# Kernel tuning notes

Hardware: AMD Instinct MI355X
Metric: run time of the kernel (lower is better)

The kernel has to match this reference:

```python
import jax, jax.numpy as jnp
import numpy as np

EPS = 1e-6


def _rmsnorm(x, w, eps=EPS):
    # x: (..., d); normalize over last dim
    ms = jnp.mean(jnp.square(x), axis=-1, keepdims=True)
    return x * jax.lax.rsqrt(ms + eps) * w


def setup_inputs() -> dict:
    key = jax.random.key(0)
    ks = jax.random.split(key, 5)
    B, S, D = 2, 2048, 2048
    n_heads, n_kv = 16, 4
    d_head = D // n_heads  # 128
    sd = 1.0 / np.sqrt(D)
    return {
        "x": jax.random.normal(ks[0], (B, S, D), dtype=jnp.float32),
        "wq": jax.random.normal(ks[1], (D, n_heads * d_head), dtype=jnp.float32) * sd,
        "wk": jax.random.normal(ks[2], (D, n_kv * d_head), dtype=jnp.float32) * sd,
        "wv": jax.random.normal(ks[3], (D, n_kv * d_head), dtype=jnp.float32) * sd,
        "wo": jax.random.normal(ks[4], (D, D), dtype=jnp.float32) * sd,
        "q_norm_w": jnp.ones((d_head,), dtype=jnp.float32),
        "k_norm_w": jnp.ones((d_head,), dtype=jnp.float32),
    }


def reference(x, wq, wk, wv, wo, q_norm_w, k_norm_w):
    B, S, D = x.shape
    n_heads, n_kv = 16, 4
    groups = n_heads // n_kv
    d_head = D // n_heads

    # QKV projections (bias=False)
    q = (x @ wq).reshape(B, S, n_kv, groups, d_head)  # q heads grouped by kv head
    k = (x @ wk).reshape(B, S, n_kv, d_head)
    v = (x @ wv).reshape(B, S, n_kv, d_head)

    # qk RMSNorm over d_head
    q = _rmsnorm(q, q_norm_w)
    k = _rmsnorm(k, k_norm_w)

    # GQA attention without materializing expanded K/V:
    # scores: (B, n_kv, groups, S_q, S_k)
    scale = 1.0 / jnp.sqrt(jnp.asarray(d_head, dtype=x.dtype))
    scores = jnp.einsum('bskgd,btkd->bkgst', q, k) * scale
    causal = jnp.tril(jnp.ones((S, S), dtype=bool))
    scores = jnp.where(causal, scores, jnp.asarray(-jnp.inf, dtype=scores.dtype))
    attn = jax.nn.softmax(scores, axis=-1)
    out = jnp.einsum('bkgst,btkd->bskgd', attn, v)  # (B, S, n_kv, groups, d_head)
    out = out.reshape(B, S, D)
    return out @ wo
```

## Files before the change

kernel.cpp:

```cpp
#include <hip/hip_runtime.h>
#include <hip/hip_bf16.h>
#include <stdint.h>

typedef unsigned short u16;
typedef __attribute__((ext_vector_type(8))) short short8;
typedef __attribute__((ext_vector_type(4))) float f32x4;
typedef __attribute__((ext_vector_type(16))) float f32x16;

__device__ __forceinline__ u16 f2bf(float f){
  union { __hip_bfloat16 h; u16 u; } v; v.h = __float2bfloat16(f); return v.u;
}
__device__ __forceinline__ float bf2f(u16 h){
  union { uint32_t u; float f; } v; v.u = ((uint32_t)h) << 16;
  return v.f;
}
__device__ __forceinline__ f32x4 mfma16(short8 a, short8 b, f32x4 c){
  return __builtin_amdgcn_mfma_f32_16x16x32_bf16(a, b, c, 0, 0, 0);
}
__device__ __forceinline__ f32x16 mfma32(short8 a, short8 b, f32x16 c){
  return __builtin_amdgcn_mfma_f32_32x32x16_bf16(a, b, c, 0, 0, 0);
}
__device__ __forceinline__ void gl_lds16(const u16* g, u16* l){
  __builtin_amdgcn_global_load_lds((const __attribute__((address_space(1))) void*)g,
                                   (__attribute__((address_space(3))) void*)l, 16, 0, 0);
}
template<int N> __device__ __forceinline__ void waitvm(){
  if constexpr (N==0) asm volatile("s_waitcnt vmcnt(0)" ::: "memory");
  else if constexpr (N==4) asm volatile("s_waitcnt vmcnt(4)" ::: "memory");
  else static_assert(N==0 || N==4, "unsupported vmcnt");
}
__device__ __forceinline__ void phase_sep(){
  __builtin_amdgcn_sched_barrier(0);
  __builtin_amdgcn_s_barrier();
  __builtin_amdgcn_sched_barrier(0);
}

__global__ __launch_bounds__(256) void cvt_x(const float* __restrict__ s,
                                             u16* __restrict__ d, int n4){
  const int i = blockIdx.x*256 + threadIdx.x;
  if (i >= n4) return;
  const float4 v = ((const float4*)s)[i];
  ushort4 pk;
  pk.x = f2bf(v.x); pk.y = f2bf(v.y); pk.z = f2bf(v.z); pk.w = f2bf(v.w);
  ((ushort4*)d)[i] = pk;
}

__global__ __launch_bounds__(256) void transpose_cvt(const float* __restrict__ src,
    u16* __restrict__ dst, int R, int C)
{
  __shared__ float tile[32][33];
  const int tx = threadIdx.x, ty = threadIdx.y;
  const int c0 = blockIdx.x << 5, r0 = blockIdx.y << 5;
  #pragma unroll
  for (int i=0;i<4;i++)
    tile[ty + (i<<3)][tx] = src[(size_t)(r0 + ty + (i<<3))*C + c0 + tx];
  __syncthreads();
  #pragma unroll
  for (int i=0;i<4;i++)
    dst[(size_t)(c0 + ty + (i<<3))*R + r0 + tx] = f2bf(tile[tx][ty + (i<<3)]);
}

__global__ __launch_bounds__(256) void v_transpose(const u16* __restrict__ qkv,
    u16* __restrict__ vT)
{
  __shared__ u16 tile[32][33];
  const int tx = threadIdx.x, ty = threadIdx.y;
  const int s0 = blockIdx.x << 5, d0 = blockIdx.y << 5;
  const int bk = blockIdx.z; const int b = bk >> 2, kv = bk & 3;
  const u16* src = qkv + (size_t)b*2048*3072 + 2560 + kv*128;
  #pragma unroll
  for (int i=0;i<4;i++)
    tile[ty + (i<<3)][tx] = src[(size_t)(s0 + ty + (i<<3))*3072 + d0 + tx];
  __syncthreads();
  u16* dst = vT + (size_t)((b<<2)+kv)*128*2048;
  #pragma unroll
  for (int i=0;i<4;i++)
    dst[(size_t)(d0 + ty + (i<<3))*2048 + s0 + tx] = tile[tx][ty + (i<<3)];
}

__global__ __launch_bounds__(256) void rmsnorm_qk(u16* __restrict__ qkv,
    const float* __restrict__ qw, const float* __restrict__ kw)
{
  const int lane = threadIdx.x & 63;
  const int rid = blockIdx.x*4 + (threadIdx.x >> 6);
  const int row = rid / 20;
  const int slot = rid % 20;
  u16* p = qkv + (size_t)row*3072 + slot*128 + (lane<<1);
  const u16 r0 = p[0], r1 = p[1];
  const float a = bf2f(r0), c = bf2f(r1);
  float ss = a*a + c*c;
  #pragma unroll
  for (int off=1; off<64; off<<=1) ss += __shfl_xor(ss, off);
  float sc = rsqrtf(ss*(1.0f/128.0f) + 1e-6f);
  if (slot < 16) sc *= 0.1275187952317199f;
  const float* wp = (slot < 16) ? qw : kw;
  const float w0 = wp[lane<<1], w1 = wp[(lane<<1)+1];
  p[0] = f2bf(a*sc*w0);
  p[1] = f2bf(c*sc*w1);
}

template<int CBF16>
__global__ __launch_bounds__(512, 2) void gemm8(const u16* __restrict__ A,
    const u16* __restrict__ BT, void* __restrict__ Cp,
    int M, int N, int K, int ldc)
{
  __shared__ u16 lds[65536];
  const int tid = threadIdx.x;
  const int w = tid >> 6, lane = tid & 63;
  const int l15 = lane & 15, lg = lane >> 4;
  const int wm = w >> 2, wn = w & 3;
  const int nbx = N >> 8;
  const int nwg = gridDim.x;
  int bid = blockIdx.x;
  bid = (bid & 7) * (nwg >> 3) + (bid >> 3);
  const int m0 = (bid / nbx) << 8;
  const int n0 = (bid % nbx) << 8;

  const u16* gA0 = A  + (size_t)m0*K;
  const u16* gA1 = gA0 + (size_t)128*K;
  const u16* gB0 = BT + (size_t)n0*K;
  const u16* gB1 = gB0 + (size_t)128*K;

  auto slot = [&](int d, int s)->u16*{ return lds + (((d<<2)+s)<<13); };

  auto stage_half = [&](const u16* gbase, int kt, u16* sbase){
    #pragma unroll
    for (int i=0;i<2;i++){
      const int p = (i<<9) + tid;
      const int row = p>>3, sg = (p&7) ^ (row&7);
      gl_lds16(gbase + (size_t)row*K + (kt<<6) + (sg<<3), sbase + (p<<3));
    }
  };
  auto frag_at = [&](const u16* buf, int lrow, int kk)->short8{
    const int s = ((kk<<2)+lg) ^ (lrow&7);
    return *(const short8*)(buf + (((lrow<<3)+s)<<3));
  };

  short8 af[4][2], bfe[2][2], bfo[2][2];
  f32x4 acc[8][4];
  #pragma unroll
  for (int m=0;m<8;m++)
    #pragma unroll
    for (int n=0;n<4;n++) acc[m][n] = (f32x4){0.f,0.f,0.f,0.f};

  const int bh = 2 + (wn>>1);
  const int brow0 = ((wn&1)<<6) + l15;

  auto rd_a = [&](const u16* buf, int mq){
    #pragma unroll
    for (int m=0;m<4;m++)
      #pragma unroll
      for (int kk=0;kk<2;kk++)
        af[m][kk] = frag_at(buf, (mq<<6) + (m<<4) + l15, kk);
  };
  auto rd_b = [&](const u16* buf, int nq, short8 (*dst)[2]){
    #pragma unroll
    for (int n=0;n<2;n++)
      #pragma unroll
      for (int kk=0;kk<2;kk++)
        dst[n][kk] = frag_at(buf, brow0 + (nq<<5) + (n<<4), kk);
  };
  auto do_mfma = [&](int mb, int nb, short8 (*bf)[2]){
    __builtin_amdgcn_s_setprio(1);
    #pragma unroll
    for (int m=0;m<4;m++)
      #pragma unroll
      for (int n=0;n<2;n++)
        #pragma unroll
        for (int kk=0;kk<2;kk++)
          acc[mb+m][nb+n] = mfma16(af[m][kk], bf[n][kk], acc[mb+m][nb+n]);
    __builtin_amdgcn_s_setprio(0);
  };

  stage_half(gA0, 0, slot(0,0)); stage_half(gA1, 0, slot(0,1));
  stage_half(gB0, 0, slot(0,2)); stage_half(gB1, 0, slot(0,3));
  stage_half(gA0, 1, slot(1,0)); stage_half(gA1, 1, slot(1,1));
  waitvm<4>();
  phase_sep();

  const int niter = K >> 7;
  for (int i=0; i<niter; ++i){
    const bool full = (i+1 < niter);
    const int t1 = 2*i+1;
    rd_a(slot(0,wm), 0); rd_b(slot(0,bh), 0, bfe);
    stage_half(gB0, t1, slot(1,2)); stage_half(gB1, t1, slot(1,3));
    phase_sep();
    do_mfma(0, 0, bfe);
    phase_sep();
    rd_b(slot(0,bh), 1, bfo);
    phase_sep();
    do_mfma(0, 2, bfo);
    phase_sep();
    rd_a(slot(0,wm), 1);
    phase_sep();
    do_mfma(4, 2, bfo);
    phase_sep();
    rd_b(slot(0,bh), 0, bfe);
    if (full){ stage_half(gA0, t1+1, slot(0,0)); stage_half(gA1, t1+1, slot(0,1)); }
    phase_sep();
    do_mfma(4, 0, bfe);
    if (full) waitvm<4>(); else waitvm<0>();
    phase_sep();
    rd_a(slot(1,wm), 0); rd_b(slot(1,bh), 0, bfe);
    if (full){ stage_half(gB0, t1+1, slot(0,2)); stage_half(gB1, t1+1, slot(0,3)); }
    phase_sep();
    do_mfma(0, 0, bfe);
    phase_sep();
    rd_b(slot(1,bh), 1, bfo);
    phase_sep();
    do_mfma(0, 2, bfo);
    phase_sep();
    rd_a(slot(1,wm), 1);
    phase_sep();
    do_mfma(4, 2, bfo);
    phase_sep();
    rd_b(slot(1,bh), 0, bfe);
    if (full){ stage_half(gA0, t1+2, slot(1,0)); stage_half(gA1, t1+2, slot(1,1)); }
    phase_sep();
    do_mfma(4, 0, bfe);
    if (full) waitvm<4>();
    phase_sep();
  }

  #pragma unroll
  for (int m=0;m<8;m++){
    #pragma unroll
    for (int n=0;n<4;n++){
      const int col = n0 + (wn<<6) + (n<<4) + l15;
      #pragma unroll
      for (int r=0;r<4;r++){
        const int row = m0 + (wm<<7) + (m<<4) + (lg<<2) + r;
        if (CBF16) ((u16*)Cp)[(size_t)row*ldc + col] = f2bf(acc[m][n][r]);
        else       ((float*)Cp)[(size_t)row*ldc + col] = acc[m][n][r];
      }
    }
  }
}

__global__ __launch_bounds__(512, 2) void attn_kernel(const u16* __restrict__ qkv,
    const u16* __restrict__ vT, u16* __restrict__ aout)
{
  __shared__ u16 Klds[2][8192];
  __shared__ u16 Vlds[2][8192];
  __shared__ u16 Plds[8][2048];
  const int tid = threadIdx.x;
  const int w = tid >> 6, lane = tid & 63;
  const int l31 = lane & 31, hi = lane >> 5;
  const int P = blockIdx.x;
  const int h = blockIdx.y, b = blockIdx.z;
  const int kvh = h >> 2;
  const int side = w >> 2, sub = w & 3;
  const int qb = (side ? P*128 : (15-P)*128) + (sub<<5);
  const int nt = 32 - 2*P;
  const int ltmax = 2*P + 1;

  const u16* qkvb = qkv + (size_t)b*2048*3072;
  short8 qf[8];
  {
    const u16* qp = qkvb + (size_t)(qb + l31)*3072 + h*128 + hi*8;
    #pragma unroll
    for (int kk=0;kk<8;kk++) qf[kk] = *(const short8*)(qp + kk*16);
  }
  f32x16 oacc[4];
  #pragma unroll
  for (int d=0;d<4;d++)
    #pragma unroll
    for (int r=0;r<16;r++) oacc[d][r] = 0.f;
  float m_run = -__builtin_inff(), lsum = 0.f;

  const u16* kb_ = qkvb + 2048 + kvh*128;
  const u16* vb_ = vT + (size_t)((b<<2)+kvh)*128*2048;

  auto stageKV = [&](int t, int buf){
    const int t0s = t<<6;
    #pragma unroll
    for (int i=0;i<2;i++){
      const int u = (i<<9) + tid;
      const int row = u>>4, d0 = (u&15) ^ (row&15);
      gl_lds16(kb_ + (size_t)(t0s+row)*3072 + (d0<<3), &Klds[buf][u<<3]);
    }
    #pragma unroll
    for (int i=0;i<2;i++){
      const int u = (i<<9) + tid;
      const int rp = u>>4, z = (u&15) ^ (rp&15);
      const int d = (rp<<1) + (z>>3), k8 = z&7;
      gl_lds16(vb_ + (size_t)d*2048 + t0s + (k8<<3), &Vlds[buf][u<<3]);
    }
  };

  u16* Pw = &Plds[w][0];
  const int prp = l31>>1;

  stageKV(0, 0);
  asm volatile("s_waitcnt vmcnt(0)" ::: "memory");
  __syncthreads();

  int cur = 0;
  for (int t=0; t<nt; ++t){
    if (t+1 < nt) stageKV(t+1, cur^1);
    const int t0 = t<<6;
    const bool active = (side ? (t <= ltmax) : true) && (t0 <= qb + 31);
    if (active){
      f32x16 s0, s1;
      #pragma unroll
      for (int r=0;r<16;r++){ s0[r] = 0.f; s1[r] = 0.f; }
      #pragma unroll
      for (int kk=0;kk<8;kk++){
        const int d0 = (kk<<1) + hi;
        const int row0 = l31,     sl0 = d0 ^ (row0&15);
        const int row1 = 32+l31,  sl1 = d0 ^ (row1&15);
        const short8 k0 = *(const short8*)&Klds[cur][((row0<<4)+sl0)<<3];
        s0 = mfma32(k0, qf[kk], s0);
        const short8 k1 = *(const short8*)&Klds[cur][((row1<<4)+sl1)<<3];
        s1 = mfma32(k1, qf[kk], s1);
      }
      if (t0 + 63 > qb){
        const int qrel = qb + l31 - t0;
        #pragma unroll
        for (int r=0;r<16;r++){
          const int kloc = (r&3) + ((r>>2)<<3) + (hi<<2);
          if (kloc      > qrel) s0[r] = -__builtin_inff();
          if (kloc + 32 > qrel) s1[r] = -__builtin_inff();
        }
      }
      float t8[8];
      #pragma unroll
      for (int i=0;i<8;i++) t8[i] = fmaxf(fmaxf(s0[i], s0[i+8]), fmaxf(s1[i], s1[i+8]));
      #pragma unroll
      for (int i=0;i<4;i++) t8[i] = fmaxf(t8[i], t8[i+4]);
      float mx = fmaxf(fmaxf(t8[0],t8[1]), fmaxf(t8[2],t8[3]));
      mx = fmaxf(mx, __shfl_xor(mx, 32));
      const bool noskip = !__all(mx - m_run <= 8.0f);
      const float mnew = noskip ? fmaxf(m_run, mx) : m_run;
      float rs = 0.f;
      #pragma unroll
      for (int i=0;i<16;i++){
        s0[i] = __builtin_amdgcn_exp2f(s0[i] - mnew);
        s1[i] = __builtin_amdgcn_exp2f(s1[i] - mnew);
        rs += s0[i] + s1[i];
      }
      rs += __shfl_xor(rs, 32);
      if (noskip){
        const float corr = __builtin_amdgcn_exp2f(m_run - mnew);
        m_run = mnew;
        lsum = lsum*corr + rs;
        #pragma unroll
        for (int r=0;r<16;r++){
          const float cr = __shfl(corr, (r&3) + ((r>>2)<<3) + (hi<<2));
          #pragma unroll
          for (int db=0;db<4;db++) oacc[db][r] *= cr;
        }
      } else {
        lsum += rs;
      }
      #pragma unroll
      for (int kb2=0;kb2<2;kb2++)
        #pragma unroll
        for (int j=0;j<4;j++){
          const int r4 = j<<2;
          uint2 v;
          if (kb2==0){
            v.x = (uint32_t)f2bf(s0[r4+0]) | ((uint32_t)f2bf(s0[r4+1])<<16);
            v.y = (uint32_t)f2bf(s0[r4+2]) | ((uint32_t)f2bf(s0[r4+3])<<16);
          } else {
            v.x = (uint32_t)f2bf(s1[r4+0]) | ((uint32_t)f2bf(s1[r4+1])<<16);
            v.y = (uint32_t)f2bf(s1[r4+2]) | ((uint32_t)f2bf(s1[r4+3])<<16);
          }
          const int sl = (((l31&1)<<3) | ((kb2<<2)+j)) ^ (prp&15);
          *(uint2*)((char*)Pw + ((((prp<<4)+sl)<<4) + (hi<<3))) = v;
        }
      asm volatile("s_waitcnt lgkmcnt(0)" ::: "memory");
      __builtin_amdgcn_sched_barrier(0);
      #pragma unroll
      for (int kk=0;kk<4;kk++){
        const int k8 = (kk<<1) + hi;
        const int slp = (((l31&1)<<3) | k8) ^ (prp&15);
        const short8 pa = *(const short8*)&Pw[((prp<<4)+slp)<<3];
        #pragma unroll
        for (int db=0;db<4;db++){
          const int d = (db<<5) + l31;
          const int rp = d>>1;
          const int slv = (((d&1)<<3) | k8) ^ (rp&15);
          const short8 vv = *(const short8*)&Vlds[cur][((rp<<4)+slv)<<3];
          oacc[db] = mfma32(pa, vv, oacc[db]);
        }
      }
    }
    asm volatile("s_waitcnt vmcnt(0)" ::: "memory");
    __syncthreads();
    cur ^= 1;
  }

  const float inv = 1.0f / lsum;
  #pragma unroll
  for (int r=0;r<16;r++){
    const int qr = (r&3) + ((r>>2)<<3) + (hi<<2);
    const float ivr = __shfl(inv, qr);
    u16* op = aout + (size_t)(b*2048 + qb + qr)*2048 + h*128 + l31;
    #pragma unroll
    for (int db=0;db<4;db++)
      op[db<<5] = f2bf(oacc[db][r] * ivr);
  }
}

extern "C" void kernel_launch(void* const* d_in, const int* in_sizes, int n_in,
                              void* d_out, int out_size, void* d_ws, size_t ws_size,
                              hipStream_t stream) {
  const float* x  = (const float*)d_in[0];
  const float* wq = (const float*)d_in[1];
  const float* wk = (const float*)d_in[2];
  const float* wv = (const float*)d_in[3];
  const float* wo = (const float*)d_in[4];
  const float* qw = (const float*)d_in[5];
  const float* kw = (const float*)d_in[6];
  char* ws = (char*)d_ws;
  u16* xbf   = (u16*)(ws);
  u16* wqkvT = (u16*)(ws + 16777216);
  u16* woT   = (u16*)(ws + 29360128);
  u16* qkv   = (u16*)(ws + 37748736);
  u16* vT    = (u16*)(ws + 62914560);
  float* out = (float*)d_out;

  dim3 tb(32,8);
  cvt_x<<<8192, 256, 0, stream>>>(x, xbf, 2097152);
  transpose_cvt<<<dim3(64,64), tb, 0, stream>>>(wq, wqkvT,             2048, 2048);
  transpose_cvt<<<dim3(16,64), tb, 0, stream>>>(wk, wqkvT + 2048*2048, 2048, 512);
  transpose_cvt<<<dim3(16,64), tb, 0, stream>>>(wv, wqkvT + 2560*2048, 2048, 512);
  transpose_cvt<<<dim3(64,64), tb, 0, stream>>>(wo, woT,               2048, 2048);
  gemm8<1><<<192, 512, 0, stream>>>(xbf, wqkvT, qkv, 4096, 3072, 2048, 3072);
  rmsnorm_qk<<<20480, 256, 0, stream>>>(qkv, qw, kw);
  v_transpose<<<dim3(64,4,8), tb, 0, stream>>>(qkv, vT);
  attn_kernel<<<dim3(8,16,2), 512, 0, stream>>>(qkv, vT, xbf);
  gemm8<0><<<128, 512, 0, stream>>>(xbf, woT, out, 4096, 2048, 2048, 2048);
}
```

Measured before the change: 215.9 us.

## Restructure attention into 256-thread blocks with register-resident P and split K/V staging

The attention kernel moves from 512-thread blocks that pair two query tiles to 256-thread blocks each owning one 128-row query tile. The grid doubles and the light/heavy ordering is flipped by batch index. The P matrix no longer round-trips through LDS. It is packed in registers with v_cvt_pk_bf16_f32 and rearranged across lanes with v_permlane32_swap to form the MFMA A operand. K stays double-buffered while V is single-buffered and loaded each tile, with staged vmcnt waits and barriers to overlap the next K load with compute. This removes LDS traffic and the lgkm wait for P, but adds an extra barrier per tile and exposes V load latency.

```diff
diff --git a/kernel.cpp b/kernel.cpp
--- a/kernel.cpp
+++ b/kernel.cpp
@@ -27,12 +27,18 @@
 template<int N> __device__ __forceinline__ void waitvm(){
   if constexpr (N==0) asm volatile("s_waitcnt vmcnt(0)" ::: "memory");
   else if constexpr (N==4) asm volatile("s_waitcnt vmcnt(4)" ::: "memory");
-  else static_assert(N==0 || N==4, "unsupported vmcnt");
+  else if constexpr (N==8) asm volatile("s_waitcnt vmcnt(8)" ::: "memory");
+  else static_assert(N==0 || N==4 || N==8, "unsupported vmcnt");
 }
 __device__ __forceinline__ void phase_sep(){
   __builtin_amdgcn_sched_barrier(0);
   __builtin_amdgcn_s_barrier();
   __builtin_amdgcn_sched_barrier(0);
+}
+__device__ __forceinline__ uint32_t cvtpk(float lo, float hi){
+  uint32_t r;
+  asm("v_cvt_pk_bf16_f32 %0, %1, %2" : "=v"(r) : "v"(lo), "v"(hi));
+  return r;
 }
 
 __global__ __launch_bounds__(256) void cvt_x(const float* __restrict__ s,
@@ -237,22 +243,19 @@
   }
 }
 
-__global__ __launch_bounds__(512, 2) void attn_kernel(const u16* __restrict__ qkv,
+__global__ __launch_bounds__(256, 2) void attn_kernel(const u16* __restrict__ qkv,
     const u16* __restrict__ vT, u16* __restrict__ aout)
 {
   __shared__ u16 Klds[2][8192];
-  __shared__ u16 Vlds[2][8192];
-  __shared__ u16 Plds[8][2048];
+  __shared__ u16 Vlds[8192];
   const int tid = threadIdx.x;
   const int w = tid >> 6, lane = tid & 63;
   const int l31 = lane & 31, hi = lane >> 5;
-  const int P = blockIdx.x;
-  const int h = blockIdx.y, b = blockIdx.z;
+  const int bx = blockIdx.x, h = blockIdx.y, b = blockIdx.z;
+  const int qI = b ? bx : (15 - bx);
   const int kvh = h >> 2;
-  const int side = w >> 2, sub = w & 3;
-  const int qb = (side ? P*128 : (15-P)*128) + (sub<<5);
-  const int nt = 32 - 2*P;
-  const int ltmax = 2*P + 1;
+  const int qb = qI*128 + (w<<5);
+  const int nt = 2*qI + 2;
 
   const u16* qkvb = qkv + (size_t)b*2048*3072;
   short8 qf[8];
@@ -271,47 +274,46 @@
   const u16* kb_ = qkvb + 2048 + kvh*128;
   const u16* vb_ = vT + (size_t)((b<<2)+kvh)*128*2048;
 
-  auto stageKV = [&](int t, int buf){
-    const int t0s = t<<6;
-    #pragma unroll
-    for (int i=0;i<2;i++){
-      const int u = (i<<9) + tid;
+  auto stageK = [&](int t, int buf){
+    #pragma unroll
+    for (int i=0;i<4;i++){
+      const int u = (i<<8) + tid;
       const int row = u>>4, d0 = (u&15) ^ (row&15);
-      gl_lds16(kb_ + (size_t)(t0s+row)*3072 + (d0<<3), &Klds[buf][u<<3]);
-    }
-    #pragma unroll
-    for (int i=0;i<2;i++){
-      const int u = (i<<9) + tid;
+      gl_lds16(kb_ + (size_t)((t<<6)+row)*3072 + (d0<<3), &Klds[buf][u<<3]);
+    }
+  };
+  auto stageV = [&](int t){
+    #pragma unroll
+    for (int i=0;i<4;i++){
+      const int u = (i<<8) + tid;
       const int rp = u>>4, z = (u&15) ^ (rp&15);
       const int d = (rp<<1) + (z>>3), k8 = z&7;
-      gl_lds16(vb_ + (size_t)d*2048 + t0s + (k8<<3), &Vlds[buf][u<<3]);
-    }
-  };
-
-  u16* Pw = &Plds[w][0];
-  const int prp = l31>>1;
-
-  stageKV(0, 0);
-  asm volatile("s_waitcnt vmcnt(0)" ::: "memory");
-  __syncthreads();
-
-  int cur = 0;
+      gl_lds16(vb_ + (size_t)d*2048 + (t<<6) + (k8<<3), &Vlds[u<<3]);
+    }
+  };
+
+  stageK(0, 0);
+  int kbuf = 0;
   for (int t=0; t<nt; ++t){
-    if (t+1 < nt) stageKV(t+1, cur^1);
+    const bool pre = (t+1 < nt);
+    stageV(t);
+    if (pre) stageK(t+1, kbuf^1);
+    if (pre) waitvm<8>(); else waitvm<4>();
+    phase_sep();
     const int t0 = t<<6;
-    const bool active = (side ? (t <= ltmax) : true) && (t0 <= qb + 31);
-    if (active){
+    const bool act = (t0 <= qb + 31);
+    uint32_t paw[4][4];
+    if (act){
       f32x16 s0, s1;
       #pragma unroll
       for (int r=0;r<16;r++){ s0[r] = 0.f; s1[r] = 0.f; }
       #pragma unroll
       for (int kk=0;kk<8;kk++){
         const int d0 = (kk<<1) + hi;
-        const int row0 = l31,     sl0 = d0 ^ (row0&15);
-        const int row1 = 32+l31,  sl1 = d0 ^ (row1&15);
-        const short8 k0 = *(const short8*)&Klds[cur][((row0<<4)+sl0)<<3];
+        const short8 k0 = *(const short8*)&Klds[kbuf][((l31<<4) + (d0 ^ (l31&15)))<<3];
         s0 = mfma32(k0, qf[kk], s0);
-        const short8 k1 = *(const short8*)&Klds[cur][((row1<<4)+sl1)<<3];
+        const int r1 = 32 + l31;
+        const short8 k1 = *(const short8*)&Klds[kbuf][((r1<<4) + (d0 ^ (r1&15)))<<3];
         s1 = mfma32(k1, qf[kk], s1);
       }
       if (t0 + 63 > qb){
@@ -354,41 +356,39 @@
         lsum += rs;
       }
       #pragma unroll
-      for (int kb2=0;kb2<2;kb2++)
-        #pragma unroll
-        for (int j=0;j<4;j++){
-          const int r4 = j<<2;
-          uint2 v;
-          if (kb2==0){
-            v.x = (uint32_t)f2bf(s0[r4+0]) | ((uint32_t)f2bf(s0[r4+1])<<16);
-            v.y = (uint32_t)f2bf(s0[r4+2]) | ((uint32_t)f2bf(s0[r4+3])<<16);
-          } else {
-            v.x = (uint32_t)f2bf(s1[r4+0]) | ((uint32_t)f2bf(s1[r4+1])<<16);
-            v.y = (uint32_t)f2bf(s1[r4+2]) | ((uint32_t)f2bf(s1[r4+3])<<16);
-          }
-          const int sl = (((l31&1)<<3) | ((kb2<<2)+j)) ^ (prp&15);
-          *(uint2*)((char*)Pw + ((((prp<<4)+sl)<<4) + (hi<<3))) = v;
-        }
-      asm volatile("s_waitcnt lgkmcnt(0)" ::: "memory");
-      __builtin_amdgcn_sched_barrier(0);
-      #pragma unroll
       for (int kk=0;kk<4;kk++){
-        const int k8 = (kk<<1) + hi;
-        const int slp = (((l31&1)<<3) | k8) ^ (prp&15);
-        const short8 pa = *(const short8*)&Pw[((prp<<4)+slp)<<3];
+        const int base = (kk&1)<<3;
+        float v0,v1,v2,v3,v4,v5,v6,v7;
+        if (kk<2){ v0=s0[base+0]; v1=s0[base+1]; v2=s0[base+2]; v3=s0[base+3];
+                   v4=s0[base+4]; v5=s0[base+5]; v6=s0[base+6]; v7=s0[base+7]; }
+        else     { v0=s1[base+0]; v1=s1[base+1]; v2=s1[base+2]; v3=s1[base+3];
+                   v4=s1[base+4]; v5=s1[base+5]; v6=s1[base+6]; v7=s1[base+7]; }
+        uint32_t a0 = cvtpk(v0, v1), a1 = cvtpk(v2, v3);
+        uint32_t b0 = cvtpk(v4, v5), b1 = cvtpk(v6, v7);
+        asm volatile("v_permlane32_swap_b32 %0, %1" : "+v"(a0), "+v"(b0));
+        asm volatile("v_permlane32_swap_b32 %0, %1" : "+v"(a1), "+v"(b1));
+        paw[kk][0] = a0; paw[kk][1] = a1; paw[kk][2] = b0; paw[kk][3] = b1;
+      }
+    }
+    if (pre) waitvm<4>(); else waitvm<0>();
+    phase_sep();
+    if (act){
+      #pragma unroll
+      for (int kk=0;kk<4;kk++){
+        union { uint32_t w[4]; short8 v; } pu;
+        pu.w[0]=paw[kk][0]; pu.w[1]=paw[kk][1]; pu.w[2]=paw[kk][2]; pu.w[3]=paw[kk][3];
+        const short8 pa = pu.v;
         #pragma unroll
         for (int db=0;db<4;db++){
-          const int d = (db<<5) + l31;
-          const int rp = d>>1;
-          const int slv = (((d&1)<<3) | k8) ^ (rp&15);
-          const short8 vv = *(const short8*)&Vlds[cur][((rp<<4)+slv)<<3];
+          const int d = (db<<5) + l31, rp = d>>1;
+          const int sl = (((d&1)<<3) | ((kk<<1)+hi)) ^ (rp&15);
+          const short8 vv = *(const short8*)&Vlds[((rp<<4)+sl)<<3];
           oacc[db] = mfma32(pa, vv, oacc[db]);
         }
       }
     }
-    asm volatile("s_waitcnt vmcnt(0)" ::: "memory");
-    __syncthreads();
-    cur ^= 1;
+    phase_sep();
+    kbuf ^= 1;
   }
 
   const float inv = 1.0f / lsum;
@@ -430,6 +430,6 @@
   gemm8<1><<<192, 512, 0, stream>>>(xbf, wqkvT, qkv, 4096, 3072, 2048, 3072);
   rmsnorm_qk<<<20480, 256, 0, stream>>>(qkv, qw, kw);
   v_transpose<<<dim3(64,4,8), tb, 0, stream>>>(qkv, vT);
-  attn_kernel<<<dim3(8,16,2), 512, 0, stream>>>(qkv, vT, xbf);
+  attn_kernel<<<dim3(16,16,2), 256, 0, stream>>>(qkv, vT, xbf);
   gemm8<0><<<128, 512, 0, stream>>>(xbf, woT, out, 4096, 2048, 2048, 2048);
 }
```

Result: no change. 214.0 us (-0.9%).
